# Performance work log

Hardware: AMD Instinct MI355X
Metric: run time of the kernel (lower is better)

Reference implementation:

```python
import jax, jax.numpy as jnp
import numpy as np

N = 50000      # nodes
E = 800000     # edges (avg degree 16)
RAW = 128      # raw_dim
HID = 256      # hidden_dim
OUT = 64       # out_dim
K = 4          # n_kernels
PHI = 16       # phi_dim
EPS = 1e-8


def setup_inputs() -> dict:
    key = jax.random.key(0)
    ks = jax.random.split(key, 8)
    h_l = jax.random.normal(ks[0], (N, HID), jnp.float32)
    e_l = jax.random.normal(ks[1], (N, RAW), jnp.float32)
    src = jax.random.randint(ks[2], (E,), 0, N, dtype=jnp.int32)
    dst = jax.random.randint(ks[3], (E,), 0, N, dtype=jnp.int32)
    gain = np.sqrt(2.0)
    W_phi = jax.random.normal(ks[4], (RAW, PHI - 1), jnp.float32) * (gain * np.sqrt(2.0 / (RAW + PHI - 1)))
    W1 = jax.random.normal(ks[5], (HID, RAW), jnp.float32) * np.sqrt(2.0 / (RAW + HID))
    b1 = jnp.zeros((HID,), jnp.float32)
    W2 = jax.random.normal(ks[6], (K * PHI, HID), jnp.float32) * np.sqrt(2.0 / (HID + K * PHI))
    b2 = jnp.zeros((K * PHI,), jnp.float32)
    tilde_phi = jnp.eye(PHI, dtype=jnp.float32)[-K:]       # n_kernels <= phi_dim branch
    W = jax.random.normal(ks[7], (HID, OUT * K), jnp.float32) * (gain * np.sqrt(2.0 / (HID + OUT * K)))
    bias = jnp.zeros((OUT,), jnp.float32)
    return {"h_l": h_l, "e_l": e_l, "src": src, "dst": dst,
            "W_phi": W_phi, "W1": W1, "b1": b1, "W2": W2, "b2": b2,
            "tilde_phi": tilde_phi, "W": W, "bias": bias}


def reference(h_l, e_l, src, dst, W_phi, W1, b1, W2, b2, tilde_phi, W, bias):
    # per-node kernelized features: [N, K, OUT]
    h = (h_l @ W).reshape(N, K, OUT)
    # pseudo-coordinates: [N, PHI-1]
    phi_k = e_l @ W_phi
    # normalized kernel anchors: [K, PHI]
    tilde_norm = tilde_phi / jnp.linalg.norm(tilde_phi, axis=1, keepdims=True)
    # deformation offsets: [N, K, PHI]
    hid = jax.nn.relu(e_l @ W1.T + b1)
    delta_k = (hid @ W2.T + b2).reshape(N, K, PHI)
    delta_ik = tilde_norm[None, :, :] + delta_k            # [N, K, PHI]

    # edge relative position (u_sub_v): [E, PHI-1]
    dist = phi_k[src] - phi_k[dst]
    mask = jnp.all(dist == 0.0, axis=1)                    # self/coincident edges
    dist = jnp.concatenate([dist, mask.astype(dist.dtype)[:, None]], axis=1)  # [E, PHI]
    dist = dist / jnp.clip(jnp.linalg.norm(dist, axis=1, keepdims=True), EPS)

    # per-edge per-kernel attention logit: a_ijk = <dist, delta_ik[dst]>  -> [E, K]
    a = jnp.einsum('ep,ekp->ek', dist, delta_ik[dst])

    # edge_softmax: softmax over incoming edges per destination node
    m = jax.ops.segment_max(a, dst, num_segments=N)        # [N, K]
    ex = jnp.exp(a - m[dst])
    s = jax.ops.segment_sum(ex, dst, num_segments=N)       # [N, K]
    att = ex / s[dst]                                      # [E, K]

    # message passing: u_mul_e then sum over incoming edges
    msg = h[src] * att[:, :, None]                         # [E, K, OUT]
    agg = jax.ops.segment_sum(msg, dst, num_segments=N)    # [N, K, OUT]

    out = agg.sum(axis=1) + bias[None, :]                  # [N, OUT]
    out = out / jnp.clip(jnp.linalg.norm(out, axis=1, keepdims=True), EPS)

    # regularizers
    d2 = ((tilde_norm[:, None, :] - tilde_norm[None, :, :]) ** 2).sum(-1)  # [K, K]
    l_sep = d2.sum() / K                                   # sum_k mean_j ||.||^2
    l_focus = (delta_k ** 2).sum(-1).mean()
    return out, l_sep, l_focus
```

## Files before the change

### kernel.cpp

```cpp
#include <hip/hip_runtime.h>
#include <math.h>

#define NN 50000
#define EE 800000

typedef __attribute__((ext_vector_type(8))) short short8;
typedef __attribute__((ext_vector_type(4))) float f32x4;
typedef __attribute__((ext_vector_type(2))) float f32x2;

__device__ inline float b2f(unsigned u16) {
    union { unsigned i; float f; } v; v.i = (u16 & 0xFFFFu) << 16; return v.f;
}
__device__ inline unsigned short f2b(float f) {
    unsigned u = __float_as_uint(f);
    unsigned r = (u + 0x7FFFu + ((u >> 16) & 1u)) >> 16;
    return (unsigned short)r;
}
__device__ inline unsigned cvt_pk_bf16(float lo, float hi) {
    unsigned r;
    asm("v_cvt_pk_bf16_f32 %0, %1, %2" : "=v"(r) : "v"(lo), "v"(hi));
    return r;
}
__device__ inline void gload16(const unsigned short* g, unsigned short* l) {
    __builtin_amdgcn_global_load_lds(
        (const __attribute__((address_space(1))) void*)g,
        (__attribute__((address_space(3))) void*)l, 16, 0, 0);
}

#define PREP_THREADS (800000 + 65536 + 32768 + 16384 + 2048)

__global__ __launch_bounds__(256) void prep_k(const float* __restrict__ W,
                                              const float* __restrict__ W1,
                                              const float* __restrict__ W2,
                                              const float* __restrict__ W_phi,
                                              const float* __restrict__ tilde_phi,
                                              const int* __restrict__ dst,
                                              unsigned short* __restrict__ W_t,
                                              unsigned short* __restrict__ W1_bf,
                                              unsigned short* __restrict__ W2_bf,
                                              unsigned short* __restrict__ Wphi_t,
                                              int* __restrict__ deg,
                                              int* __restrict__ rank,
                                              float* __restrict__ tnorm,
                                              float* __restrict__ lsep_out) {
    if (blockIdx.x == 0) {
        __shared__ float tn[64];
        int t = threadIdx.x;
        if (t < 64) {
            float v = tilde_phi[t];
            float sq = v * v;
            #pragma unroll
            for (int s = 8; s; s >>= 1) sq += __shfl_xor(sq, s, 16);
            float tnv = v / sqrtf(sq);
            tn[t] = tnv;
            tnorm[t] = tnv;
        }
        __syncthreads();
        if (t == 0) {
            float tot = 0.f;
            for (int a = 0; a < 4; ++a)
                for (int b = 0; b < 4; ++b) {
                    float s2 = 0.f;
                    for (int p = 0; p < 16; ++p) {
                        float df = tn[a * 16 + p] - tn[b * 16 + p];
                        s2 += df * df;
                    }
                    tot += s2;
                }
            lsep_out[0] = tot * 0.25f;
        }
    }
    int i = blockIdx.x * 256 + threadIdx.x;
    if (i < 800000) {
        rank[i] = atomicAdd(&deg[dst[i]], 1);
    } else if (i < 865536) {
        int j = i - 800000;
        int cp = j >> 8, r = j & 255;
        int b = (cp & ~63) | ((cp & 15) * 4) | ((cp >> 4) & 3);
        int ch = b >> 2, k = b & 3;
        W_t[j] = f2b(W[(size_t)r * 256 + (k << 6) + ch]);
    } else if (i < 898304) {
        int j = i - 865536;
        W1_bf[j] = f2b(W1[j]);
    } else if (i < 914688) {
        int j = i - 898304;
        W2_bf[j] = f2b(W2[j]);
    } else if (i < 916736) {
        int j = i - 914688;
        int cp = j >> 7, r = j & 127;
        Wphi_t[j] = (cp < 15) ? f2b(W_phi[(size_t)r * 15 + cp]) : (unsigned short)0;
    }
}

__device__ __forceinline__ void hgemm8_body(unsigned short* lds,
                                            const float* __restrict__ A,
                                            const unsigned short* __restrict__ Bt,
                                            unsigned int* __restrict__ h8w,
                                            int bxm, int bxn) {
    unsigned short* As = lds;
    unsigned short* Bs = lds + 4096;
    const int tid = threadIdx.x;
    const int l = tid & 63, l15 = l & 15, l4 = l >> 4;
    const int w = tid >> 6;
    const int wr = w >> 1, wc = w & 1;
    const int row0 = bxm * 128, col0 = bxn * 128;
    const int wrow = wr * 32, wcol = wc * 64;

    auto stage = [&](int k0) {
        {
            int o = tid, r = o >> 2, s = o & 3;
            int gr = row0 + r; if (gr >= NN) gr = NN - 1;
            const float* Af = A + (size_t)gr * 256 + k0 + s * 8;
            float4 f0 = *(const float4*)Af, f1 = *(const float4*)(Af + 4);
            *(uint4*)&As[o * 8] = make_uint4(cvt_pk_bf16(f0.x, f0.y), cvt_pk_bf16(f0.z, f0.w),
                                             cvt_pk_bf16(f1.x, f1.y), cvt_pk_bf16(f1.z, f1.w));
        }
        {
            int o = tid, r = o >> 2, s = o & 3;
            gload16(&Bt[(size_t)(col0 + r) * 256 + k0 + s * 8], &Bs[(o - l) * 8]);
        }
    };

    f32x4 acc[2][4];
    #pragma unroll
    for (int m = 0; m < 2; ++m)
        #pragma unroll
        for (int n = 0; n < 4; ++n) acc[m][n] = (f32x4){0.f, 0.f, 0.f, 0.f};

    stage(0);
    for (int t = 0; t < 8; ++t) {
        __syncthreads();
        short8 af[2], bfr[4];
        #pragma unroll
        for (int m = 0; m < 2; ++m)
            af[m] = *(const short8*)&As[((wrow + m * 16 + l15) * 4 + l4) * 8];
        #pragma unroll
        for (int n = 0; n < 4; ++n)
            bfr[n] = *(const short8*)&Bs[((wcol + n * 16 + l15) * 4 + l4) * 8];
        #pragma unroll
        for (int m = 0; m < 2; ++m)
            #pragma unroll
            for (int n = 0; n < 4; ++n)
                acc[m][n] = __builtin_amdgcn_mfma_f32_16x16x32_bf16(af[m], bfr[n], acc[m][n], 0, 0, 0);
        if (t + 1 < 8) { __syncthreads(); stage((t + 1) * 32); }
    }
    #pragma unroll
    for (int m = 0; m < 2; ++m)
        #pragma unroll
        for (int r = 0; r < 4; ++r) {
            int gr = row0 + wrow + m * 16 + l4 * 4 + r;
            if (gr >= NN) continue;
            unsigned pk = __builtin_amdgcn_cvt_pk_fp8_f32(acc[m][0][r], acc[m][1][r], 0, false);
            pk = __builtin_amdgcn_cvt_pk_fp8_f32(acc[m][2][r], acc[m][3][r], pk, true);
            h8w[(size_t)gr * 64 + ((col0 + wcol) >> 2) + l15] = pk;
        }
}

#define LDPAD 264

__device__ __forceinline__ void hiddelta_body(unsigned short* lds,
                                              const float* __restrict__ e_l,
                                              const unsigned short* __restrict__ W1_bf,
                                              const unsigned short* __restrict__ Wphi_t,
                                              const unsigned short* __restrict__ W2_bf,
                                              const float* __restrict__ b1,
                                              const float* __restrict__ b2,
                                              const float* __restrict__ tnorm,
                                              float* __restrict__ phi,
                                              float* __restrict__ deltap,
                                              float* __restrict__ lf_part, int bxm) {
    unsigned short* As = lds;
    unsigned short* Bs = lds + 2048;
    unsigned short* Wp = lds + 10240;
    unsigned short* hidL = lds;
    const int tid = threadIdx.x;
    const int l = tid & 63, l15 = l & 15, l4 = l >> 4;
    const int w = tid >> 6;
    const int wr = w >> 1, wc = w & 1;
    const int row0 = bxm * 64;

    if (tid < 256) gload16(&Wphi_t[tid * 8], &Wp[(tid - l) * 8]);

    auto stage = [&](int k0) {
        if (tid < 256) {
            int o = tid, r = o >> 2, s = o & 3;
            int gr = row0 + r; if (gr >= NN) gr = NN - 1;
            const float* Af = e_l + (size_t)gr * 128 + k0 + s * 8;
            float4 f0 = *(const float4*)Af, f1 = *(const float4*)(Af + 4);
            *(uint4*)&As[o * 8] = make_uint4(cvt_pk_bf16(f0.x, f0.y), cvt_pk_bf16(f0.z, f0.w),
                                             cvt_pk_bf16(f1.x, f1.y), cvt_pk_bf16(f1.z, f1.w));
        }
        #pragma unroll
        for (int o = tid; o < 1024; o += 512) {
            int r = o >> 2, s = o & 3;
            gload16(&W1_bf[(size_t)r * 128 + k0 + s * 8], &Bs[(o - l) * 8]);
        }
    };

    f32x4 acc[8], pacc;
    #pragma unroll
    for (int n = 0; n < 8; ++n) acc[n] = (f32x4){0.f, 0.f, 0.f, 0.f};
    pacc = (f32x4){0.f, 0.f, 0.f, 0.f};

    stage(0);
    for (int t = 0; t < 4; ++t) {
        int k0 = t * 32;
        __syncthreads();
        short8 af = *(const short8*)&As[((wr * 16 + l15) * 4 + l4) * 8];
        short8 bfr[8];
        #pragma unroll
        for (int n = 0; n < 8; ++n)
            bfr[n] = *(const short8*)&Bs[((wc * 128 + n * 16 + l15) * 4 + l4) * 8];
        #pragma unroll
        for (int n = 0; n < 8; ++n)
            acc[n] = __builtin_amdgcn_mfma_f32_16x16x32_bf16(af, bfr[n], acc[n], 0, 0, 0);
        if (wc == 1) {
            short8 pf = *(const short8*)&Wp[l15 * 128 + k0 + l4 * 8];
            pacc = __builtin_amdgcn_mfma_f32_16x16x32_bf16(af, pf, pacc, 0, 0, 0);
        }
        if (t + 1 < 4) { __syncthreads(); stage((t + 1) * 32); }
    }

    __syncthreads();
    #pragma unroll
    for (int n = 0; n < 8; ++n) {
        int col = wc * 128 + n * 16 + l15;
        float bv = b1[col];
        #pragma unroll
        for (int r = 0; r < 4; ++r) {
            int row = wr * 16 + l4 * 4 + r;
            hidL[row * LDPAD + col] = f2b(fmaxf(acc[n][r] + bv, 0.f));
        }
    }
    if (wc == 1) {
        #pragma unroll
        for (int r = 0; r < 4; ++r) {
            int gr = row0 + wr * 16 + l4 * 4 + r;
            if (gr < NN) phi[(size_t)gr * 16 + l15] = pacc[r];
        }
    }
    __syncthreads();

    f32x4 acc2[2];
    acc2[0] = (f32x4){0.f, 0.f, 0.f, 0.f};
    acc2[1] = (f32x4){0.f, 0.f, 0.f, 0.f};
    for (int kk = 0; kk < 8; ++kk) {
        int k0 = kk * 32;
        short8 a2 = *(const short8*)&hidL[(wr * 16 + l15) * LDPAD + k0 + l4 * 8];
        #pragma unroll
        for (int n = 0; n < 2; ++n) {
            int col = wc * 32 + n * 16 + l15;
            short8 b2f_ = *(const short8*)&W2_bf[(size_t)col * 256 + k0 + l4 * 8];
            acc2[n] = __builtin_amdgcn_mfma_f32_16x16x32_bf16(a2, b2f_, acc2[n], 0, 0, 0);
        }
    }
    float lf = 0.f;
    #pragma unroll
    for (int n = 0; n < 2; ++n) {
        int gc = wc * 32 + n * 16 + l15;
        float bv = b2[gc], tv = tnorm[gc];
        #pragma unroll
        for (int r = 0; r < 4; ++r) {
            int gr = row0 + wr * 16 + l4 * 4 + r;
            if (gr < NN) {
                float v = acc2[n][r] + bv;
                lf += v * v;
                deltap[(size_t)gr * 64 + gc] = v + tv;
            }
        }
    }
    #pragma unroll
    for (int s = 32; s; s >>= 1) lf += __shfl_xor(lf, s);
    __syncthreads();
    float* red = (float*)&lds[16896];
    if (l == 0) red[w] = lf;
    __syncthreads();
    if (tid == 0) {
        float t_ = 0.f;
        #pragma unroll
        for (int j = 0; j < 8; ++j) t_ += red[j];
        lf_part[bxm] = t_;
    }
}

__global__ __launch_bounds__(512) void fused3_k(const float* __restrict__ e_l,
                                                const float* __restrict__ h_l,
                                                const unsigned short* __restrict__ W1_bf,
                                                const unsigned short* __restrict__ Wphi_t,
                                                const unsigned short* __restrict__ W_t,
                                                const unsigned short* __restrict__ W2_bf,
                                                const float* __restrict__ b1,
                                                const float* __restrict__ b2,
                                                const float* __restrict__ tnorm,
                                                float* __restrict__ phi,
                                                unsigned int* __restrict__ h8w,
                                                float* __restrict__ deltap,
                                                float* __restrict__ lf_part,
                                                const int* __restrict__ src,
                                                const int* __restrict__ dst,
                                                const int* __restrict__ rank,
                                                const int* __restrict__ offs,
                                                unsigned short* __restrict__ csr_src) {
    __shared__ __align__(16) unsigned short lds[17408];
    int bx = blockIdx.x;
    if (bx < 391) {
        int base = bx * 2048 + threadIdx.x;
        int pos[4], sv[4];
        #pragma unroll
        for (int j = 0; j < 4; ++j) {
            int e = base + j * 512;
            if (e < EE) { pos[j] = offs[dst[e]] + rank[e]; sv[j] = src[e]; }
            else pos[j] = -1;
        }
        #pragma unroll
        for (int j = 0; j < 4; ++j)
            if (pos[j] >= 0) csr_src[pos[j]] = (unsigned short)sv[j];
    } else if (bx < 1173) {
        int b = bx - 391;
        hgemm8_body(lds, h_l, W_t, h8w, b >> 1, b & 1);
    } else {
        hiddelta_body(lds, e_l, W1_bf, Wphi_t, W2_bf, b1, b2, tnorm,
                      phi, deltap, lf_part, bx - 1173);
    }
}

#define SCAN_NB ((NN + 255) / 256)
#define LF_NB 782

__global__ __launch_bounds__(256) void scan_partial_k(const int* __restrict__ deg,
                                                      int* __restrict__ bsum) {
    __shared__ int ws_[4];
    int i = blockIdx.x * 256 + threadIdx.x;
    int v = (i < NN) ? deg[i] : 0;
    int x = v;
    #pragma unroll
    for (int s = 32; s; s >>= 1) x += __shfl_xor(x, s);
    if ((threadIdx.x & 63) == 0) ws_[threadIdx.x >> 6] = x;
    __syncthreads();
    if (threadIdx.x == 0) bsum[blockIdx.x] = ws_[0] + ws_[1] + ws_[2] + ws_[3];
}

__global__ __launch_bounds__(256) void scan_bsum_k(int* __restrict__ bsum) {
    __shared__ int sd[256];
    int t = threadIdx.x;
    int v = (t < SCAN_NB) ? bsum[t] : 0;
    sd[t] = v;
    __syncthreads();
    for (int s = 1; s < 256; s <<= 1) {
        int u = (t >= s) ? sd[t - s] : 0;
        __syncthreads();
        sd[t] += u;
        __syncthreads();
    }
    if (t < SCAN_NB) bsum[t] = sd[t] - v;
}

__global__ __launch_bounds__(256) void scan_scatter_k(const int* __restrict__ deg,
                                                      const int* __restrict__ bsum,
                                                      int* __restrict__ offs,
                                                      unsigned short* __restrict__ csr_dst) {
    __shared__ int wexc[4];
    int i = blockIdx.x * 256 + threadIdx.x;
    int lane = threadIdx.x & 63, wid = threadIdx.x >> 6;
    int v = (i < NN) ? deg[i] : 0;
    int x = v;
    #pragma unroll
    for (int d = 1; d < 64; d <<= 1) { int u = __shfl_up(x, d); if (lane >= d) x += u; }
    if (lane == 63) wexc[wid] = x;
    __syncthreads();
    if (threadIdx.x == 0) {
        int a = wexc[0], b = wexc[1], c = wexc[2];
        wexc[0] = 0; wexc[1] = a; wexc[2] = a + b; wexc[3] = a + b + c;
    }
    __syncthreads();
    int excl = (x - v) + wexc[wid] + bsum[blockIdx.x];
    if (i < NN) {
        offs[i + 1] = excl + v;
        if (i == 0) offs[0] = 0;
        for (int q = excl; q < excl + v; ++q) csr_dst[q] = (unsigned short)i;
    }
}

__global__ __launch_bounds__(256) void edge_w_k(const unsigned short* __restrict__ csr_src,
                                                const unsigned short* __restrict__ csr_dst,
                                                const float* __restrict__ phi,
                                                const float* __restrict__ deltap,
                                                uint2* __restrict__ csr_wb,
                                                const float* __restrict__ lfocus_part,
                                                float* __restrict__ lfocus_out) {
    if (blockIdx.x == 3125) {
        __shared__ float red[4];
        float s = 0.f;
        for (int i = threadIdx.x; i < LF_NB; i += 256) s += lfocus_part[i];
        #pragma unroll
        for (int st = 32; st; st >>= 1) s += __shfl_xor(s, st);
        if ((threadIdx.x & 63) == 0) red[threadIdx.x >> 6] = s;
        __syncthreads();
        if (threadIdx.x == 0)
            lfocus_out[0] = (red[0] + red[1] + red[2] + red[3]) * (1.f / ((float)NN * 4));
        return;
    }
    int e = blockIdx.x * 256 + threadIdx.x;
    if (e >= EE) return;
    int s = csr_src[e], d = csr_dst[e];
    const float4* ps4 = (const float4*)(phi + (size_t)s * 16);
    const float4* pd4 = (const float4*)(phi + (size_t)d * 16);
    float dv[16];
    float nrm2 = 0.f;
    #pragma unroll
    for (int q = 0; q < 4; ++q) {
        float4 a = ps4[q], b = pd4[q];
        dv[q * 4 + 0] = a.x - b.x;
        dv[q * 4 + 1] = a.y - b.y;
        dv[q * 4 + 2] = a.z - b.z;
        dv[q * 4 + 3] = a.w - b.w;
    }
    #pragma unroll
    for (int p = 0; p < 15; ++p) nrm2 += dv[p] * dv[p];
    float z = (nrm2 == 0.f) ? 1.f : 0.f;
    dv[15] = z;
    nrm2 += z;
    float inv = 1.f / fmaxf(sqrtf(nrm2), 1e-8f);
    const float* dl = deltap + (size_t)d * 64;
    float res[4];
    #pragma unroll
    for (int k = 0; k < 4; ++k) {
        const float4* dk = (const float4*)(dl + k * 16);
        float sacc = 0.f;
        #pragma unroll
        for (int q = 0; q < 4; ++q) {
            float4 tv = dk[q];
            sacc += dv[q * 4 + 0] * tv.x;
            sacc += dv[q * 4 + 1] * tv.y;
            sacc += dv[q * 4 + 2] * tv.z;
            sacc += dv[q * 4 + 3] * tv.w;
        }
        res[k] = __expf(sacc * inv);
    }
    csr_wb[e] = make_uint2(cvt_pk_bf16(res[0], res[1]), cvt_pk_bf16(res[2], res[3]));
}

__global__ __launch_bounds__(256) void aggregate_k(const int* __restrict__ offs,
                                                   const unsigned short* __restrict__ csr_src,
                                                   const unsigned int* __restrict__ csr_wu,
                                                   const unsigned int* __restrict__ h8,
                                                   const float* __restrict__ bias,
                                                   float* __restrict__ out) {
    int wave = threadIdx.x >> 6;
    int lane = threadIdx.x & 63;
    int n = blockIdx.x * 4 + wave;
    if (n >= NN) return;
    int beg = offs[n], end = offs[n + 1];

    float pA = 0.f, pB = 0.f;
    for (int q = beg * 2 + lane; q < end * 2; q += 64) {
        unsigned u = csr_wu[q];
        pA += b2f(u);
        pB += b2f(u >> 16);
    }
    #pragma unroll
    for (int s = 2; s < 64; s <<= 1) { pA += __shfl_xor(pA, s); pB += __shfl_xor(pB, s); }
    float iA = (pA > 0.f) ? 1.f / pA : 0.f;
    float iB = (pB > 0.f) ? 1.f / pB : 0.f;
    float i0 = __shfl(iA, 0), i1 = __shfl(iB, 0);
    float i2 = __shfl(iA, 1), i3 = __shfl(iB, 1);

    const uint2* csr_w2 = (const uint2*)csr_wu;
    float a0 = 0.f, a1 = 0.f, a2 = 0.f, a3 = 0.f;
    int p = beg;
    for (; p + 3 < end; p += 4) {
        uint2 u0 = csr_w2[p], u1 = csr_w2[p + 1], u2 = csr_w2[p + 2], u3 = csr_w2[p + 3];
        int s0 = csr_src[p], s1 = csr_src[p + 1], s2 = csr_src[p + 2], s3 = csr_src[p + 3];
        unsigned hv0 = h8[(size_t)s0 * 64 + lane];
        unsigned hv1 = h8[(size_t)s1 * 64 + lane];
        unsigned hv2 = h8[(size_t)s2 * 64 + lane];
        unsigned hv3 = h8[(size_t)s3 * 64 + lane];
        f32x2 lo, hi;
        lo = __builtin_amdgcn_cvt_pk_f32_fp8(hv0, false);
        hi = __builtin_amdgcn_cvt_pk_f32_fp8(hv0, true);
        a0 += b2f(u0.x) * lo.x; a1 += b2f(u0.x >> 16) * lo.y;
        a2 += b2f(u0.y) * hi.x; a3 += b2f(u0.y >> 16) * hi.y;
        lo = __builtin_amdgcn_cvt_pk_f32_fp8(hv1, false);
        hi = __builtin_amdgcn_cvt_pk_f32_fp8(hv1, true);
        a0 += b2f(u1.x) * lo.x; a1 += b2f(u1.x >> 16) * lo.y;
        a2 += b2f(u1.y) * hi.x; a3 += b2f(u1.y >> 16) * hi.y;
        lo = __builtin_amdgcn_cvt_pk_f32_fp8(hv2, false);
        hi = __builtin_amdgcn_cvt_pk_f32_fp8(hv2, true);
        a0 += b2f(u2.x) * lo.x; a1 += b2f(u2.x >> 16) * lo.y;
        a2 += b2f(u2.y) * hi.x; a3 += b2f(u2.y >> 16) * hi.y;
        lo = __builtin_amdgcn_cvt_pk_f32_fp8(hv3, false);
        hi = __builtin_amdgcn_cvt_pk_f32_fp8(hv3, true);
        a0 += b2f(u3.x) * lo.x; a1 += b2f(u3.x >> 16) * lo.y;
        a2 += b2f(u3.y) * hi.x; a3 += b2f(u3.y >> 16) * hi.y;
    }
    for (; p < end; ++p) {
        uint2 uA = csr_w2[p];
        int sA = csr_src[p];
        unsigned hv = h8[(size_t)sA * 64 + lane];
        f32x2 lo = __builtin_amdgcn_cvt_pk_f32_fp8(hv, false);
        f32x2 hi = __builtin_amdgcn_cvt_pk_f32_fp8(hv, true);
        a0 += b2f(uA.x) * lo.x; a1 += b2f(uA.x >> 16) * lo.y;
        a2 += b2f(uA.y) * hi.x; a3 += b2f(uA.y >> 16) * hi.y;
    }
    float v = a0 * i0 + a1 * i1 + a2 * i2 + a3 * i3 + bias[lane];
    float nr = v * v;
    #pragma unroll
    for (int s = 32; s; s >>= 1) nr += __shfl_xor(nr, s);
    float invn = 1.f / fmaxf(sqrtf(nr), 1e-8f);
    out[(size_t)n * 64 + lane] = v * invn;
}

extern "C" void kernel_launch(void* const* d_in, const int* in_sizes, int n_in,
                              void* d_out, int out_size, void* d_ws, size_t ws_size,
                              hipStream_t stream) {
    const float* h_l       = (const float*)d_in[0];
    const float* e_l       = (const float*)d_in[1];
    const int*   src       = (const int*)d_in[2];
    const int*   dst       = (const int*)d_in[3];
    const float* W_phi     = (const float*)d_in[4];
    const float* W1        = (const float*)d_in[5];
    const float* b1        = (const float*)d_in[6];
    const float* W2        = (const float*)d_in[7];
    const float* b2        = (const float*)d_in[8];
    const float* tilde_phi = (const float*)d_in[9];
    const float* W         = (const float*)d_in[10];
    const float* bias      = (const float*)d_in[11];
    float* out = (float*)d_out;
    float* lsep_ptr   = out + (size_t)NN * 64;
    float* lfocus_ptr = out + (size_t)NN * 64 + 1;

    char* ws = (char*)d_ws;
    size_t off = 0;
    auto alloc = [&](size_t bytes) -> char* {
        char* p = ws + off;
        off += (bytes + 255) & ~(size_t)255;
        return p;
    };
    float*          phi     = (float*)alloc((size_t)NN * 16 * 4);
    float*          deltap  = (float*)alloc((size_t)NN * 64 * 4);
    unsigned int*   h8w     = (unsigned int*)alloc((size_t)NN * 256);
    unsigned short* csr_src = (unsigned short*)alloc((size_t)EE * 2);
    unsigned short* csr_dst = (unsigned short*)alloc((size_t)EE * 2);
    int*            rank    = (int*)alloc((size_t)EE * 4);
    uint2*          csr_wb  = (uint2*)alloc((size_t)EE * 8);
    int*            deg     = (int*)alloc((size_t)NN * 4);
    int*            offs    = (int*)alloc((size_t)(NN + 1) * 4);
    int*            bsum    = (int*)alloc((size_t)SCAN_NB * 4);
    float*          lf_part = (float*)alloc((size_t)LF_NB * 4);
    unsigned short* W_t     = (unsigned short*)alloc(256 * 256 * 2);
    unsigned short* W1_bf   = (unsigned short*)alloc(256 * 128 * 2);
    unsigned short* W2_bf   = (unsigned short*)alloc(64 * 256 * 2);
    unsigned short* Wphi_t  = (unsigned short*)alloc(16 * 128 * 2);
    float*          tnorm   = (float*)alloc(64 * 4);

    hipMemsetAsync(deg, 0, (size_t)NN * 4, stream);

    prep_k<<<(PREP_THREADS + 255) / 256, 256, 0, stream>>>(
        W, W1, W2, W_phi, tilde_phi, dst,
        W_t, W1_bf, W2_bf, Wphi_t, deg, rank, tnorm, lsep_ptr);

    scan_partial_k<<<SCAN_NB, 256, 0, stream>>>(deg, bsum);
    scan_bsum_k<<<1, 256, 0, stream>>>(bsum);
    scan_scatter_k<<<SCAN_NB, 256, 0, stream>>>(deg, bsum, offs, csr_dst);

    fused3_k<<<1955, 512, 0, stream>>>(e_l, h_l, W1_bf, Wphi_t, W_t, W2_bf,
                                       b1, b2, tnorm, phi, h8w, deltap, lf_part,
                                       src, dst, rank, offs, csr_src);

    edge_w_k<<<3126, 256, 0, stream>>>(csr_src, csr_dst, phi, deltap, csr_wb,
                                       lf_part, lfocus_ptr);

    aggregate_k<<<12500, 256, 0, stream>>>(offs, csr_src, (const unsigned int*)csr_wb,
                                           h8w, bias, out);
}
```

Baseline: 166.6 us.

## Double-buffer h GEMM staging, store delta in bf16, reorder fused block roles

The h_l@W GEMM body now uses two LDS buffers, so the next K-slice is staged while MFMAs run on the current one, with one barrier per iteration instead of two. The per-node deformation offsets (deltap) are stored as bf16 instead of fp32, which halves the gather traffic in the edge-weight kernel at some cost in precision. The block-index ranges in the fused kernel are reordered so the GEMM and hid/delta blocks dispatch before the CSR scatter blocks.

```diff
diff --git a/kernel.cpp b/kernel.cpp
--- a/kernel.cpp
+++ b/kernel.cpp
@@ -98,7 +98,7 @@
                                             unsigned int* __restrict__ h8w,
                                             int bxm, int bxn) {
     unsigned short* As = lds;
-    unsigned short* Bs = lds + 4096;
+    unsigned short* Bs = lds + 8192;
     const int tid = threadIdx.x;
     const int l = tid & 63, l15 = l & 15, l4 = l >> 4;
     const int w = tid >> 6;
@@ -106,19 +106,17 @@
     const int row0 = bxm * 128, col0 = bxn * 128;
     const int wrow = wr * 32, wcol = wc * 64;
 
-    auto stage = [&](int k0) {
-        {
-            int o = tid, r = o >> 2, s = o & 3;
-            int gr = row0 + r; if (gr >= NN) gr = NN - 1;
-            const float* Af = A + (size_t)gr * 256 + k0 + s * 8;
-            float4 f0 = *(const float4*)Af, f1 = *(const float4*)(Af + 4);
-            *(uint4*)&As[o * 8] = make_uint4(cvt_pk_bf16(f0.x, f0.y), cvt_pk_bf16(f0.z, f0.w),
-                                             cvt_pk_bf16(f1.x, f1.y), cvt_pk_bf16(f1.z, f1.w));
-        }
-        {
-            int o = tid, r = o >> 2, s = o & 3;
-            gload16(&Bt[(size_t)(col0 + r) * 256 + k0 + s * 8], &Bs[(o - l) * 8]);
-        }
+    const int r_ = tid >> 2, s_ = tid & 3;
+    int gr_ = row0 + r_; if (gr_ >= NN) gr_ = NN - 1;
+
+    auto stage = [&](int buf, int k0) {
+        const float* Af = A + (size_t)gr_ * 256 + k0 + s_ * 8;
+        float4 f0 = *(const float4*)Af, f1 = *(const float4*)(Af + 4);
+        *(uint4*)&As[buf * 4096 + tid * 8] =
+            make_uint4(cvt_pk_bf16(f0.x, f0.y), cvt_pk_bf16(f0.z, f0.w),
+                       cvt_pk_bf16(f1.x, f1.y), cvt_pk_bf16(f1.z, f1.w));
+        gload16(&Bt[(size_t)(col0 + r_) * 256 + k0 + s_ * 8],
+                &Bs[buf * 4096 + (tid - l) * 8]);
     };
 
     f32x4 acc[2][4];
@@ -127,22 +125,25 @@
         #pragma unroll
         for (int n = 0; n < 4; ++n) acc[m][n] = (f32x4){0.f, 0.f, 0.f, 0.f};
 
-    stage(0);
+    stage(0, 0);
+    __syncthreads();
+    int cur = 0;
     for (int t = 0; t < 8; ++t) {
-        __syncthreads();
+        if (t + 1 < 8) stage(cur ^ 1, (t + 1) * 32);
         short8 af[2], bfr[4];
         #pragma unroll
         for (int m = 0; m < 2; ++m)
-            af[m] = *(const short8*)&As[((wrow + m * 16 + l15) * 4 + l4) * 8];
+            af[m] = *(const short8*)&As[cur * 4096 + ((wrow + m * 16 + l15) * 4 + l4) * 8];
         #pragma unroll
         for (int n = 0; n < 4; ++n)
-            bfr[n] = *(const short8*)&Bs[((wcol + n * 16 + l15) * 4 + l4) * 8];
+            bfr[n] = *(const short8*)&Bs[cur * 4096 + ((wcol + n * 16 + l15) * 4 + l4) * 8];
         #pragma unroll
         for (int m = 0; m < 2; ++m)
             #pragma unroll
             for (int n = 0; n < 4; ++n)
                 acc[m][n] = __builtin_amdgcn_mfma_f32_16x16x32_bf16(af[m], bfr[n], acc[m][n], 0, 0, 0);
-        if (t + 1 < 8) { __syncthreads(); stage((t + 1) * 32); }
+        if (t + 1 < 8) __syncthreads();
+        cur ^= 1;
     }
     #pragma unroll
     for (int m = 0; m < 2; ++m)
@@ -167,7 +168,7 @@
                                               const float* __restrict__ b2,
                                               const float* __restrict__ tnorm,
                                               float* __restrict__ phi,
-                                              float* __restrict__ deltap,
+                                              unsigned short* __restrict__ deltap,
                                               float* __restrict__ lf_part, int bxm) {
     unsigned short* As = lds;
     unsigned short* Bs = lds + 2048;
@@ -265,7 +266,7 @@
             if (gr < NN) {
                 float v = acc2[n][r] + bv;
                 lf += v * v;
-                deltap[(size_t)gr * 64 + gc] = v + tv;
+                deltap[(size_t)gr * 64 + gc] = f2b(v + tv);
             }
         }
     }
@@ -294,7 +295,7 @@
                                                 const float* __restrict__ tnorm,
                                                 float* __restrict__ phi,
                                                 unsigned int* __restrict__ h8w,
-                                                float* __restrict__ deltap,
+                                                unsigned short* __restrict__ deltap,
                                                 float* __restrict__ lf_part,
                                                 const int* __restrict__ src,
                                                 const int* __restrict__ dst,
@@ -303,8 +304,13 @@
                                                 unsigned short* __restrict__ csr_src) {
     __shared__ __align__(16) unsigned short lds[17408];
     int bx = blockIdx.x;
-    if (bx < 391) {
-        int base = bx * 2048 + threadIdx.x;
+    if (bx < 782) {
+        hgemm8_body(lds, h_l, W_t, h8w, bx >> 1, bx & 1);
+    } else if (bx < 1564) {
+        hiddelta_body(lds, e_l, W1_bf, Wphi_t, W2_bf, b1, b2, tnorm,
+                      phi, deltap, lf_part, bx - 782);
+    } else {
+        int base = (bx - 1564) * 2048 + threadIdx.x;
         int pos[4], sv[4];
         #pragma unroll
         for (int j = 0; j < 4; ++j) {
@@ -315,12 +321,6 @@
         #pragma unroll
         for (int j = 0; j < 4; ++j)
             if (pos[j] >= 0) csr_src[pos[j]] = (unsigned short)sv[j];
-    } else if (bx < 1173) {
-        int b = bx - 391;
-        hgemm8_body(lds, h_l, W_t, h8w, b >> 1, b & 1);
-    } else {
-        hiddelta_body(lds, e_l, W1_bf, Wphi_t, W2_bf, b1, b2, tnorm,
-                      phi, deltap, lf_part, bx - 1173);
     }
 }
 
@@ -384,7 +384,7 @@
 __global__ __launch_bounds__(256) void edge_w_k(const unsigned short* __restrict__ csr_src,
                                                 const unsigned short* __restrict__ csr_dst,
                                                 const float* __restrict__ phi,
-                                                const float* __restrict__ deltap,
+                                                const unsigned short* __restrict__ deltap,
                                                 uint2* __restrict__ csr_wb,
                                                 const float* __restrict__ lfocus_part,
                                                 float* __restrict__ lfocus_out) {
@@ -421,19 +421,16 @@
     dv[15] = z;
     nrm2 += z;
     float inv = 1.f / fmaxf(sqrtf(nrm2), 1e-8f);
-    const float* dl = deltap + (size_t)d * 64;
+    const uint2* dl2 = (const uint2*)(deltap + (size_t)d * 64);
     float res[4];
     #pragma unroll
     for (int k = 0; k < 4; ++k) {
-        const float4* dk = (const float4*)(dl + k * 16);
         float sacc = 0.f;
         #pragma unroll
         for (int q = 0; q < 4; ++q) {
-            float4 tv = dk[q];
-            sacc += dv[q * 4 + 0] * tv.x;
-            sacc += dv[q * 4 + 1] * tv.y;
-            sacc += dv[q * 4 + 2] * tv.z;
-            sacc += dv[q * 4 + 3] * tv.w;
+            uint2 u = dl2[k * 4 + q];
+            sacc += dv[q * 4 + 0] * b2f(u.x) + dv[q * 4 + 1] * b2f(u.x >> 16)
+                  + dv[q * 4 + 2] * b2f(u.y) + dv[q * 4 + 3] * b2f(u.y >> 16);
         }
         res[k] = __expf(sacc * inv);
     }
@@ -537,7 +534,7 @@
         return p;
     };
     float*          phi     = (float*)alloc((size_t)NN * 16 * 4);
-    float*          deltap  = (float*)alloc((size_t)NN * 64 * 4);
+    unsigned short* deltap  = (unsigned short*)alloc((size_t)NN * 64 * 2);
     unsigned int*   h8w     = (unsigned int*)alloc((size_t)NN * 256);
     unsigned short* csr_src = (unsigned short*)alloc((size_t)EE * 2);
     unsigned short* csr_dst = (unsigned short*)alloc((size_t)EE * 2);
```

Result: no change. 164.4 us (-1.3%).
